# Optimization experiments

Hardware: AMD Instinct MI355X
Metric: run time of the kernel (lower is better)

Reference implementation:

```python
import jax, jax.numpy as jnp
import numpy as np

B, S, P = 64, 1024, 1024
D_IN, D, OUT = 50, 300, 1024
LN_EPS = 1e-6  # custom LayerNorm in repo-style code (a_2/b_2, eps=1e-6)


def setup_inputs() -> dict:
    key = jax.random.key(0)
    ks = jax.random.split(key, 16)
    std = 1e-4  # matches torch .normal_(mean=0, std=0.0001)
    return {
        "x": jax.random.normal(ks[0], (B, S, D_IN), jnp.float32),
        "matrix_embed": jax.random.normal(ks[1], (D_IN, D), jnp.float32),
        "past": jax.random.normal(ks[2], (B, P, D_IN), jnp.float32),
        "w_pt": jax.random.normal(ks[3], (D_IN, D), jnp.float32) * std,
        "b_pt": jax.random.normal(ks[4], (1, D), jnp.float32) * std,
        "w_pg": jax.random.normal(ks[5], (D_IN, D), jnp.float32) * std,
        "b_pg": jax.random.normal(ks[6], (1, D), jnp.float32) * std,
        "w_ps": jax.random.normal(ks[7], (D_IN, D), jnp.float32) * std,
        "b_ps": jax.random.normal(ks[8], (1, D), jnp.float32) * std,
        "w_ex": jax.random.normal(ks[9], (D_IN, D), jnp.float32) * std,
        "b_ex": jax.random.normal(ks[10], (1, D), jnp.float32) * std,
        "ln_g": jnp.ones((D,), jnp.float32),
        "ln_b": jnp.zeros((D,), jnp.float32),
        "W1": jax.random.normal(ks[11], (D, D), jnp.float32) * 0.05,
        "b1": jnp.zeros((D,), jnp.float32),
        "W2": jax.random.normal(ks[12], (D, OUT), jnp.float32) * 0.05,
        "b2": jnp.zeros((OUT,), jnp.float32),
    }


def _layernorm(h, g, b):
    mu = jnp.mean(h, axis=-1, keepdims=True)
    var = jnp.mean(jnp.square(h - mu), axis=-1, keepdims=True)
    return g * (h - mu) / jnp.sqrt(var + LN_EPS) + b


def reference(x, matrix_embed, past, w_pt, b_pt, w_pg, b_pg, w_ps, b_ps,
              w_ex, b_ex, ln_g, ln_b, W1, b1, W2, b2):
    # token: [B,S,300]
    token = _layernorm(x @ matrix_embed, ln_g, ln_b)
    past_token = jnp.tanh(x @ w_pt + b_pt)          # [B,S,300]
    past_vector = jnp.tanh(past @ w_pg + b_pg)      # [B,P,300]
    past_gate = jax.nn.sigmoid(jnp.einsum('bsd,bpd->bsp', past_token, past_vector))
    past_state = jnp.tanh(past @ w_ps + b_ps)       # [B,P,300]
    pre_state = past_gate @ past_state              # [B,S,300]
    expose_vector = jnp.tanh(x @ w_ex + b_ex)       # [B,S,300]
    expose_gate = jax.nn.sigmoid(jnp.einsum('bsd,btd->bst', expose_vector, pre_state))
    filter_token = token + expose_gate @ pre_state  # [B,S,300]
    # output MLP (dropout is identity in eval mode)
    h = jax.nn.relu(filter_token @ W1 + b1)
    return h @ W2 + b2
```

## Files before the change

kernel.cpp:

```cpp
#include <hip/hip_runtime.h>
#include <hip/hip_bf16.h>
#include <math.h>

typedef __attribute__((ext_vector_type(8))) short bf16x8;
typedef __attribute__((ext_vector_type(4))) float f32x4;

__device__ inline float bf2f(short u) {
  union { float f; unsigned int i; } v;
  v.i = ((unsigned int)(unsigned short)u) << 16;
  return v.f;
}
__device__ inline short f2bf(float f) {
  union { float f; unsigned int i; } v; v.f = f;
  unsigned int r = v.i + 0x7fff + ((v.i >> 16) & 1);
  return (short)(r >> 16);
}

__global__ void pad_rows(const float* __restrict__ src, short* __restrict__ dst,
                         int C, int Cp, int total) {
  int i = blockIdx.x * 256 + threadIdx.x;
  if (i >= total) return;
  int r = i / Cp, c = i - r * Cp;
  dst[i] = f2bf(c < C ? src[(size_t)r * C + c] : 0.f);
}

__global__ void pad_T(const float* __restrict__ src, short* __restrict__ dst,
                      int K, int N, int Kp, int total) {
  int i = blockIdx.x * 256 + threadIdx.x;
  if (i >= total) return;
  int n = i / Kp, k = i - n * Kp;
  dst[i] = f2bf((k < K && n < N) ? src[(size_t)k * N + n] : 0.f);
}

__global__ __launch_bounds__(256) void transpose_pd(const short* __restrict__ in,
                                                    short* __restrict__ out) {
  __shared__ unsigned int T[64][32];
  const int b = blockIdx.z, p0 = blockIdx.x * 64, d0 = blockIdx.y * 64;
  const short* ib = in + (size_t)b * 1024 * 320;
  short* ob = out + (size_t)b * 320 * 1024;
  for (int i = threadIdx.x; i < 512; i += 256) {
    int p = i >> 3, g = i & 7;
    uint4 v = *(const uint4*)&ib[(size_t)(p0 + p) * 320 + d0 + g * 8];
    int s = p & 31;
    T[p][(4 * g + 0) ^ s] = v.x;
    T[p][(4 * g + 1) ^ s] = v.y;
    T[p][(4 * g + 2) ^ s] = v.z;
    T[p][(4 * g + 3) ^ s] = v.w;
  }
  __syncthreads();
  for (int i = threadIdx.x; i < 512; i += 256) {
    int d = i >> 3, g = i & 7;
    int w0 = d >> 1;
    __align__(16) unsigned short tmp[8];
#pragma unroll
    for (int j = 0; j < 8; ++j) {
      int p = g * 8 + j;
      unsigned int val = T[p][w0 ^ (p & 31)];
      tmp[j] = (d & 1) ? (unsigned short)(val >> 16) : (unsigned short)(val & 0xffff);
    }
    *(uint4*)&ob[(size_t)(d0 + d) * 1024 + p0 + g * 8] = *(const uint4*)tmp;
  }
}

template<int NT, int MODE>
__global__ __launch_bounds__(512) void gemm_ep(
    const short* __restrict__ A, const short* __restrict__ Bt, int K,
    const float* __restrict__ bias, int biasN,
    void* __restrict__ outp, int outStride)
{
  __shared__ __align__(16) short Bst[NT][40];
  const int tid = threadIdx.x;
  const int wave = tid >> 6, lane = tid & 63;
  const int m = lane & 15, quad = lane >> 4;
  const int row0 = blockIdx.x * 128 + wave * 16;
  const int n0 = blockIdx.y * NT;

  f32x4 zero = {0.f, 0.f, 0.f, 0.f};
  f32x4 acc[NT / 16];
#pragma unroll
  for (int i = 0; i < NT / 16; ++i) acc[i] = zero;

  const short* arow = A + (size_t)(row0 + m) * K;

  for (int k0 = 0; k0 < K; k0 += 32) {
    __syncthreads();
    for (int idx = tid; idx < NT * 4; idx += 512) {
      int n = idx >> 2, kc = (idx & 3) << 3;
      *(uint4*)&Bst[n][kc] = *(const uint4*)&Bt[(size_t)(n0 + n) * K + k0 + kc];
    }
    __syncthreads();
    bf16x8 af = *(const bf16x8*)(arow + k0 + quad * 8);
#pragma unroll
    for (int nt = 0; nt < NT / 16; ++nt) {
      bf16x8 bf = *(const bf16x8*)&Bst[nt * 16 + m][quad * 8];
      acc[nt] = __builtin_amdgcn_mfma_f32_16x16x32_bf16(af, bf, acc[nt], 0, 0, 0);
    }
  }

#pragma unroll
  for (int nt = 0; nt < NT / 16; ++nt) {
#pragma unroll
    for (int r = 0; r < 4; ++r) {
      int row = row0 + quad * 4 + r;
      int col = n0 + nt * 16 + m;
      float v = acc[nt][r];
      if (MODE != 0) v += (col < biasN) ? bias[col] : 0.f;
      if (MODE == 1) v = tanhf(v);
      if (MODE == 2) v = fmaxf(v, 0.f);
      if (MODE == 3)
        ((float*)outp)[(size_t)row * outStride + col] = v;
      else
        ((short*)outp)[(size_t)row * outStride + col] = f2bf(v);
    }
  }
}

__global__ __launch_bounds__(256) void ln_rows(short* __restrict__ tp,
                                               const float* __restrict__ g,
                                               const float* __restrict__ bb) {
  const int wave = threadIdx.x >> 6, lane = threadIdx.x & 63;
  const int row = blockIdx.x * 4 + wave;
  short* p = tp + (size_t)row * 320;
  float vals[5], s = 0.f, ss = 0.f;
#pragma unroll
  for (int i = 0; i < 5; ++i) {
    int c = lane + i * 64;
    float v = (c < 300) ? bf2f(p[c]) : 0.f;
    vals[i] = v; s += v; ss += v * v;
  }
#pragma unroll
  for (int off = 32; off > 0; off >>= 1) { s += __shfl_down(s, off); ss += __shfl_down(ss, off); }
  s = __shfl(s, 0); ss = __shfl(ss, 0);
  const float mu = s * (1.f / 300.f);
  const float rstd = rsqrtf(ss * (1.f / 300.f) - mu * mu + 1e-6f);
#pragma unroll
  for (int i = 0; i < 5; ++i) {
    int c = lane + i * 64;
    float v = (c < 300) ? (g[c] * (vals[i] - mu) * rstd + bb[c]) : 0.f;
    p[c] = f2bf(v);
  }
}

__device__ inline void gload16(const short* g, short* l) {
  __builtin_amdgcn_global_load_lds((const __attribute__((address_space(1))) void*)g,
                                   (__attribute__((address_space(3))) void*)l, 16, 0, 0);
}
__device__ inline void block_sync() {
  asm volatile("s_waitcnt vmcnt(0) lgkmcnt(0)" ::: "memory");
  __builtin_amdgcn_s_barrier();
  __builtin_amdgcn_sched_barrier(0);
}

__global__ __launch_bounds__(512, 2) void attn_v3(
    const short* __restrict__ Qm, const short* __restrict__ Km,
    const short* __restrict__ VT, const short* __restrict__ tokp,
    short* __restrict__ Outp)
{
  __shared__ __align__(16) short KsL[2][10240];
  __shared__ __align__(16) short VsL[2][10240];
  __shared__ __align__(16) short PsL[2][5120];

  const int tid = threadIdx.x;
  const int wave = tid >> 6, lane = tid & 63;
  const int m = lane & 15, quad = lane >> 4;
  const int b = blockIdx.x;
  const int qrow0 = b * 1024 + blockIdx.y * 128;
  const size_t kbase = (size_t)b * 1024 * 320;
  const short* vtb = VT + (size_t)b * 320 * 1024;

  const short* sp[5];
#pragma unroll
  for (int j = 0; j < 5; ++j) {
    int c = tid + j * 512;
    if (c < 1280) {
      int p = c / 40, ch = c - p * 40;
      sp[j] = Km + kbase + (size_t)p * 320 + (ch ^ ((p & 1) << 2)) * 8;
    } else {
      int cv = c - 1280;
      sp[j] = vtb + (size_t)(cv >> 2) * 1024 + (cv & 3) * 8;
    }
  }

  auto stage = [&](int pt) {
#pragma unroll
    for (int j = 0; j < 5; ++j) {
      int cb = j * 512 + (wave << 6);
      if (cb < 1280) {
        if (pt < 31)
          gload16(sp[j] + (size_t)(pt + 1) * 10240, &KsL[(pt + 1) & 1][cb * 8]);
      } else {
        gload16(sp[j] + pt * 32, &VsL[pt & 1][(cb - 1280) * 8]);
      }
    }
  };

#pragma unroll
  for (int j = 0; j < 3; ++j) {
    int cb = j * 512 + (wave << 6);
    if (cb < 1280) gload16(sp[j], &KsL[0][cb * 8]);
  }
  block_sync();

  if (wave < 4) {
    bf16x8 qf[2][10];
    const short* qb = Qm + (size_t)(qrow0 + wave * 32 + m) * 320;
#pragma unroll
    for (int h = 0; h < 2; ++h)
#pragma unroll
      for (int c = 0; c < 10; ++c)
        qf[h][c] = *(const bf16x8*)(qb + h * 5120 + c * 32 + quad * 8);
    const int par = m & 1;

    for (int pt = 0; pt < 32; ++pt) {
      stage(pt);
      const short* Kc = &KsL[pt & 1][0];
      f32x4 s00 = {0.f, 0.f, 0.f, 0.f}, s01 = s00, s10 = s00, s11 = s00;
      __builtin_amdgcn_s_setprio(1);
#pragma unroll
      for (int c = 0; c < 10; ++c) {
        int cc = c ^ par;
        bf16x8 b0 = *(const bf16x8*)&Kc[m * 320 + cc * 32 + quad * 8];
        bf16x8 b1 = *(const bf16x8*)&Kc[(m + 16) * 320 + cc * 32 + quad * 8];
        s00 = __builtin_amdgcn_mfma_f32_16x16x32_bf16(qf[0][c], b0, s00, 0, 0, 0);
        s10 = __builtin_amdgcn_mfma_f32_16x16x32_bf16(qf[1][c], b0, s10, 0, 0, 0);
        s01 = __builtin_amdgcn_mfma_f32_16x16x32_bf16(qf[0][c], b1, s01, 0, 0, 0);
        s11 = __builtin_amdgcn_mfma_f32_16x16x32_bf16(qf[1][c], b1, s11, 0, 0, 0);
      }
      __builtin_amdgcn_s_setprio(0);
      short* Pb = &PsL[pt & 1][0];
#pragma unroll
      for (int h = 0; h < 2; ++h) {
        const int qt = wave * 2 + h;
#pragma unroll
        for (int g = 0; g < 2; ++g) {
          f32x4 sv = h ? (g ? s11 : s10) : (g ? s01 : s00);
#pragma unroll
          for (int r = 0; r < 4; ++r) {
            float v = 1.f / (1.f + __expf(-sv[r]));
            Pb[qt * 640 + (quad * 4 + r) * 40 + g * 16 + m] = f2bf(v);
          }
        }
      }
      block_sync();
    }
  } else {
    const int ds = wave - 4;
    f32x4 zero = {0.f, 0.f, 0.f, 0.f};
    f32x4 o[8][5];
#pragma unroll
    for (int i = 0; i < 8; ++i)
#pragma unroll
      for (int j = 0; j < 5; ++j) o[i][j] = zero;

    auto pv_step = [&](int t) {
      const short* Vc = &VsL[t & 1][0];
      const short* Pr = &PsL[t & 1][0];
      bf16x8 vb[5];
#pragma unroll
      for (int u = 0; u < 5; ++u)
        vb[u] = *(const bf16x8*)&Vc[(ds * 80 + u * 16 + m) * 32 + quad * 8];
      __builtin_amdgcn_s_setprio(1);
#pragma unroll
      for (int qt = 0; qt < 8; ++qt) {
        bf16x8 pa = *(const bf16x8*)&Pr[qt * 640 + m * 40 + quad * 8];
#pragma unroll
        for (int u = 0; u < 5; ++u)
          o[qt][u] = __builtin_amdgcn_mfma_f32_16x16x32_bf16(pa, vb[u], o[qt][u], 0, 0, 0);
      }
      __builtin_amdgcn_s_setprio(0);
    };

    for (int pt = 0; pt < 32; ++pt) {
      stage(pt);
      if (pt > 0) pv_step(pt - 1);
      block_sync();
    }
    pv_step(31);

#pragma unroll
    for (int qt = 0; qt < 8; ++qt)
#pragma unroll
      for (int u = 0; u < 5; ++u)
#pragma unroll
        for (int r = 0; r < 4; ++r) {
          const size_t row = (size_t)qrow0 + qt * 16 + quad * 4 + r;
          const int col = ds * 80 + u * 16 + m;
          float v = o[qt][u][r];
          if (tokp) v += bf2f(tokp[row * 320 + col]);
          Outp[row * 320 + col] = f2bf(v);
        }
  }
}

extern "C" void kernel_launch(void* const* d_in, const int* in_sizes, int n_in,
                              void* d_out, int out_size, void* d_ws, size_t ws_size,
                              hipStream_t stream)
{
  const float* x    = (const float*)d_in[0];
  const float* me   = (const float*)d_in[1];
  const float* past = (const float*)d_in[2];
  const float* wpt  = (const float*)d_in[3];
  const float* bpt  = (const float*)d_in[4];
  const float* wpg  = (const float*)d_in[5];
  const float* bpg  = (const float*)d_in[6];
  const float* wps  = (const float*)d_in[7];
  const float* bps  = (const float*)d_in[8];
  const float* wex  = (const float*)d_in[9];
  const float* bex  = (const float*)d_in[10];
  const float* lng  = (const float*)d_in[11];
  const float* lnb  = (const float*)d_in[12];
  const float* W1   = (const float*)d_in[13];
  const float* b1   = (const float*)d_in[14];
  const float* W2   = (const float*)d_in[15];
  const float* b2   = (const float*)d_in[16];
  float* out = (float*)d_out;

  char* ws = (char*)d_ws;
  size_t off = 0;
  auto alloc = [&](size_t bytes) -> char* {
    char* p = ws + off; off += (bytes + 255) & ~(size_t)255; return p;
  };
  const size_t RB = 65536ull;
  short* xp    = (short*)alloc(RB * 64 * 2);
  short* pastp = (short*)alloc(RB * 64 * 2);
  short* wmeT  = (short*)alloc(320 * 64 * 2);
  short* wptT  = (short*)alloc(320 * 64 * 2);
  short* wpgT  = (short*)alloc(320 * 64 * 2);
  short* wpsT  = (short*)alloc(320 * 64 * 2);
  short* wexT  = (short*)alloc(320 * 64 * 2);
  short* w1T   = (short*)alloc(320 * 320 * 2);
  short* w2T   = (short*)alloc(1024ull * 320 * 2);
  short* buf0  = (short*)alloc(RB * 320 * 2);
  short* buf1  = (short*)alloc(RB * 320 * 2);
  short* buf2  = (short*)alloc(RB * 320 * 2);
  short* buf3  = (short*)alloc(RB * 320 * 2);
  short* vtbuf = (short*)alloc(RB * 320 * 2);

  {
    int total = 65536 * 64;
    pad_rows<<<dim3((total + 255) / 256), 256, 0, stream>>>(x, xp, 50, 64, total);
    pad_rows<<<dim3((total + 255) / 256), 256, 0, stream>>>(past, pastp, 50, 64, total);
  }
  {
    int t = 320 * 64;
    dim3 g((t + 255) / 256);
    pad_T<<<g, 256, 0, stream>>>(me,  wmeT, 50, 300, 64, t);
    pad_T<<<g, 256, 0, stream>>>(wpt, wptT, 50, 300, 64, t);
    pad_T<<<g, 256, 0, stream>>>(wpg, wpgT, 50, 300, 64, t);
    pad_T<<<g, 256, 0, stream>>>(wps, wpsT, 50, 300, 64, t);
    pad_T<<<g, 256, 0, stream>>>(wex, wexT, 50, 300, 64, t);
  }
  { int t = 320 * 320;  pad_T<<<(t + 255) / 256, 256, 0, stream>>>(W1, w1T, 300, 300, 320, t); }
  { int t = 1024 * 320; pad_T<<<(t + 255) / 256, 256, 0, stream>>>(W2, w2T, 300, 1024, 320, t); }

  dim3 g512(512, 1);
  dim3 tgrid(16, 5, 64);
  gemm_ep<320, 1><<<g512, 512, 0, stream>>>(xp,    wptT, 64, bpt, 300, buf0, 320);
  gemm_ep<320, 1><<<g512, 512, 0, stream>>>(pastp, wpgT, 64, bpg, 300, buf1, 320);
  gemm_ep<320, 1><<<g512, 512, 0, stream>>>(pastp, wpsT, 64, bps, 300, buf2, 320);
  transpose_pd<<<tgrid, 256, 0, stream>>>(buf2, vtbuf);

  attn_v3<<<dim3(64, 8), 512, 0, stream>>>(buf0, buf1, vtbuf, nullptr, buf3);

  gemm_ep<320, 0><<<g512, 512, 0, stream>>>(xp, wmeT, 64, nullptr, 0, buf1, 320);
  ln_rows<<<16384, 256, 0, stream>>>(buf1, lng, lnb);
  gemm_ep<320, 1><<<g512, 512, 0, stream>>>(xp, wexT, 64, bex, 300, buf2, 320);

  transpose_pd<<<tgrid, 256, 0, stream>>>(buf3, vtbuf);

  attn_v3<<<dim3(64, 8), 512, 0, stream>>>(buf2, buf3, vtbuf, buf1, buf0);

  gemm_ep<320, 2><<<g512, 512, 0, stream>>>(buf0, w1T, 320, b1, 300, buf3, 320);
  gemm_ep<256, 3><<<dim3(512, 4), 512, 0, stream>>>(buf3, w2T, 320, b2, 1024, out, 1024);
}
```

Before: 1.092 ms.

## Restructure attention kernel into 256-thread blocks with direct V loads

The attention kernel now uses 256-thread blocks covering 64 query rows instead of 512 threads covering 128 rows, doubling the grid. V is no longer staged through shared memory: PV waves read V tiles straight from global memory into registers, and each of the two PV waves owns 160 output columns instead of 80. K staging moves from all waves to the PV waves alone. This cuts LDS use per block, which should allow more resident blocks, at the cost of redundant K/V traffic across twice as many blocks and uncoalesced global V reads inside the inner loop.

Result: faster. 1.052 ms (-3.6%).

```diff
diff --git a/kernel.cpp b/kernel.cpp
--- a/kernel.cpp
+++ b/kernel.cpp
@@ -151,57 +151,23 @@
   __builtin_amdgcn_sched_barrier(0);
 }
 
-__global__ __launch_bounds__(512, 2) void attn_v3(
+__global__ __launch_bounds__(256, 2) void attn_v4(
     const short* __restrict__ Qm, const short* __restrict__ Km,
     const short* __restrict__ VT, const short* __restrict__ tokp,
     short* __restrict__ Outp)
 {
   __shared__ __align__(16) short KsL[2][10240];
-  __shared__ __align__(16) short VsL[2][10240];
-  __shared__ __align__(16) short PsL[2][5120];
+  __shared__ __align__(16) short PsL[2][2560];
 
   const int tid = threadIdx.x;
   const int wave = tid >> 6, lane = tid & 63;
   const int m = lane & 15, quad = lane >> 4;
   const int b = blockIdx.x;
-  const int qrow0 = b * 1024 + blockIdx.y * 128;
+  const int qrow0 = b * 1024 + blockIdx.y * 64;
   const size_t kbase = (size_t)b * 1024 * 320;
   const short* vtb = VT + (size_t)b * 320 * 1024;
 
-  const short* sp[5];
-#pragma unroll
-  for (int j = 0; j < 5; ++j) {
-    int c = tid + j * 512;
-    if (c < 1280) {
-      int p = c / 40, ch = c - p * 40;
-      sp[j] = Km + kbase + (size_t)p * 320 + (ch ^ ((p & 1) << 2)) * 8;
-    } else {
-      int cv = c - 1280;
-      sp[j] = vtb + (size_t)(cv >> 2) * 1024 + (cv & 3) * 8;
-    }
-  }
-
-  auto stage = [&](int pt) {
-#pragma unroll
-    for (int j = 0; j < 5; ++j) {
-      int cb = j * 512 + (wave << 6);
-      if (cb < 1280) {
-        if (pt < 31)
-          gload16(sp[j] + (size_t)(pt + 1) * 10240, &KsL[(pt + 1) & 1][cb * 8]);
-      } else {
-        gload16(sp[j] + pt * 32, &VsL[pt & 1][(cb - 1280) * 8]);
-      }
-    }
-  };
-
-#pragma unroll
-  for (int j = 0; j < 3; ++j) {
-    int cb = j * 512 + (wave << 6);
-    if (cb < 1280) gload16(sp[j], &KsL[0][cb * 8]);
-  }
-  block_sync();
-
-  if (wave < 4) {
+  if (wave < 2) {
     bf16x8 qf[2][10];
     const short* qb = Qm + (size_t)(qrow0 + wave * 32 + m) * 320;
 #pragma unroll
@@ -211,8 +177,9 @@
         qf[h][c] = *(const bf16x8*)(qb + h * 5120 + c * 32 + quad * 8);
     const int par = m & 1;
 
+    block_sync();
+
     for (int pt = 0; pt < 32; ++pt) {
-      stage(pt);
       const short* Kc = &KsL[pt & 1][0];
       f32x4 s00 = {0.f, 0.f, 0.f, 0.f}, s01 = s00, s10 = s00, s11 = s00;
       __builtin_amdgcn_s_setprio(1);
@@ -237,57 +204,75 @@
 #pragma unroll
           for (int r = 0; r < 4; ++r) {
             float v = 1.f / (1.f + __expf(-sv[r]));
-            Pb[qt * 640 + (quad * 4 + r) * 40 + g * 16 + m] = f2bf(v);
+            Pb[(qt * 16 + quad * 4 + r) * 40 + g * 16 + m] = f2bf(v);
           }
         }
       }
       block_sync();
     }
   } else {
-    const int ds = wave - 4;
+    const int v = wave - 2;
+    const short* spk[10];
+#pragma unroll
+    for (int s = 0; s < 10; ++s) {
+      int c = (v * 10 + s) * 64 + lane;
+      int p = c / 40, ch = c - p * 40;
+      spk[s] = Km + kbase + (size_t)p * 320 + (ch ^ ((p & 1) << 2)) * 8;
+    }
+    const short* vtB = vtb + (size_t)(v * 160 + m) * 1024 + quad * 8;
+
     f32x4 zero = {0.f, 0.f, 0.f, 0.f};
-    f32x4 o[8][5];
-#pragma unroll
-    for (int i = 0; i < 8; ++i)
-#pragma unroll
-      for (int j = 0; j < 5; ++j) o[i][j] = zero;
+    f32x4 o[4][10];
+#pragma unroll
+    for (int i = 0; i < 4; ++i)
+#pragma unroll
+      for (int j = 0; j < 10; ++j) o[i][j] = zero;
+
+    auto stageK = [&](int pt) {
+#pragma unroll
+      for (int s = 0; s < 10; ++s)
+        gload16(spk[s] + (size_t)pt * 10240, &KsL[pt & 1][(v * 10 + s) * 64 * 8]);
+    };
 
     auto pv_step = [&](int t) {
-      const short* Vc = &VsL[t & 1][0];
       const short* Pr = &PsL[t & 1][0];
-      bf16x8 vb[5];
-#pragma unroll
-      for (int u = 0; u < 5; ++u)
-        vb[u] = *(const bf16x8*)&Vc[(ds * 80 + u * 16 + m) * 32 + quad * 8];
+      bf16x8 pa[4];
+#pragma unroll
+      for (int qt = 0; qt < 4; ++qt)
+        pa[qt] = *(const bf16x8*)&Pr[(qt * 16 + m) * 40 + quad * 8];
+      const short* vp = vtB + t * 32;
       __builtin_amdgcn_s_setprio(1);
 #pragma unroll
-      for (int qt = 0; qt < 8; ++qt) {
-        bf16x8 pa = *(const bf16x8*)&Pr[qt * 640 + m * 40 + quad * 8];
-#pragma unroll
-        for (int u = 0; u < 5; ++u)
-          o[qt][u] = __builtin_amdgcn_mfma_f32_16x16x32_bf16(pa, vb[u], o[qt][u], 0, 0, 0);
+      for (int dt = 0; dt < 10; ++dt) {
+        bf16x8 vb = *(const bf16x8*)(vp + dt * 16384);
+#pragma unroll
+        for (int qt = 0; qt < 4; ++qt)
+          o[qt][dt] = __builtin_amdgcn_mfma_f32_16x16x32_bf16(pa[qt], vb, o[qt][dt], 0, 0, 0);
       }
       __builtin_amdgcn_s_setprio(0);
     };
 
+    stageK(0);
+    block_sync();
+
     for (int pt = 0; pt < 32; ++pt) {
-      stage(pt);
+      if (pt < 31) stageK(pt + 1);
       if (pt > 0) pv_step(pt - 1);
       block_sync();
     }
     pv_step(31);
 
 #pragma unroll
-    for (int qt = 0; qt < 8; ++qt)
-#pragma unroll
-      for (int u = 0; u < 5; ++u)
+    for (int qt = 0; qt < 4; ++qt)
+#pragma unroll
+      for (int dt = 0; dt < 10; ++dt)
 #pragma unroll
         for (int r = 0; r < 4; ++r) {
           const size_t row = (size_t)qrow0 + qt * 16 + quad * 4 + r;
-          const int col = ds * 80 + u * 16 + m;
-          float v = o[qt][u][r];
-          if (tokp) v += bf2f(tokp[row * 320 + col]);
-          Outp[row * 320 + col] = f2bf(v);
+          const int col = v * 160 + dt * 16 + m;
+          float val = o[qt][dt][r];
+          if (tokp) val += bf2f(tokp[row * 320 + col]);
+          Outp[row * 320 + col] = f2bf(val);
         }
   }
 }
@@ -360,7 +345,7 @@
   gemm_ep<320, 1><<<g512, 512, 0, stream>>>(pastp, wpsT, 64, bps, 300, buf2, 320);
   transpose_pd<<<tgrid, 256, 0, stream>>>(buf2, vtbuf);
 
-  attn_v3<<<dim3(64, 8), 512, 0, stream>>>(buf0, buf1, vtbuf, nullptr, buf3);
+  attn_v4<<<dim3(64, 16), 256, 0, stream>>>(buf0, buf1, vtbuf, nullptr, buf3);
 
   gemm_ep<320, 0><<<g512, 512, 0, stream>>>(xp, wmeT, 64, nullptr, 0, buf1, 320);
   ln_rows<<<16384, 256, 0, stream>>>(buf1, lng, lnb);
@@ -368,7 +353,7 @@
 
   transpose_pd<<<tgrid, 256, 0, stream>>>(buf3, vtbuf);
 
-  attn_v3<<<dim3(64, 8), 512, 0, stream>>>(buf2, buf3, vtbuf, buf1, buf0);
+  attn_v4<<<dim3(64, 16), 256, 0, stream>>>(buf2, buf3, vtbuf, buf1, buf0);
 
   gemm_ep<320, 2><<<g512, 512, 0, stream>>>(buf0, w1T, 320, b1, 300, buf3, 320);
   gemm_ep<256, 3><<<dim3(512, 4), 512, 0, stream>>>(buf3, w2T, 320, b2, 1024, out, 1024);
```
